# Kernel optimization log

Measured on AMD Instinct MI355X. Metric: run time of the kernel, lower is better.

## Reference

```python
import jax, jax.numpy as jnp
import numpy as np
from jax import lax

B = 4096
SRC = 50   # source_seq_len (encoder runs SRC-1 steps)
TGT = 25   # target_seq_len
R = 1024   # rnn_size
H = 67     # HUMAN_SIZE
I = 82     # input_size = 67 + 15 one-hot actions


def gru_cell(x, h, Wi, Wh, bi, bh):
    # torch.nn.GRUCell semantics; gate order (r, z, n); Wi:[3R,in], Wh:[3R,R]
    gi = x @ Wi.T + bi
    gh = h @ Wh.T + bh
    ir, iz, inn = jnp.split(gi, 3, axis=1)
    hr, hz, hn = jnp.split(gh, 3, axis=1)
    r = jax.nn.sigmoid(ir + hr)
    z = jax.nn.sigmoid(iz + hz)
    n = jnp.tanh(inn + r * hn)
    return (1.0 - z) * n + z * h


def setup_inputs() -> dict:
    key = jax.random.key(0)
    ks = jax.random.split(key, 12)
    s = 0.05
    return {
        "encoder_inputs": jax.random.normal(ks[0], (B, SRC - 1, I), jnp.float32),
        "decoder_inputs": jax.random.normal(ks[1], (B, TGT, I), jnp.float32),
        "Wi1": jax.random.normal(ks[2], (3 * R, I), jnp.float32) * s,
        "Wh1": jax.random.normal(ks[3], (3 * R, R), jnp.float32) * s,
        "bi1": jax.random.normal(ks[4], (3 * R,), jnp.float32) * s,
        "bh1": jax.random.normal(ks[5], (3 * R,), jnp.float32) * s,
        "Wi2": jax.random.normal(ks[6], (3 * R, R), jnp.float32) * s,
        "Wh2": jax.random.normal(ks[7], (3 * R, R), jnp.float32) * s,
        "bi2": jax.random.normal(ks[8], (3 * R,), jnp.float32) * s,
        "bh2": jax.random.normal(ks[9], (3 * R,), jnp.float32) * s,
        "Wfc": jax.random.normal(ks[10], (H, 2 * R), jnp.float32) * s,
        "bfc": jax.random.normal(ks[11], (H,), jnp.float32) * s,
        "use_cuda": 0,
    }


def reference(encoder_inputs, decoder_inputs, Wi1, Wh1, bi1, bh1,
              Wi2, Wh2, bi2, bh2, Wfc, bfc, use_cuda):
    # dropout=0.0 / eval mode -> dropout is identity (faithful to module defaults)
    bsz = encoder_inputs.shape[0]
    enc = jnp.transpose(encoder_inputs, (1, 0, 2))  # [SRC-1, B, I]
    dec = jnp.transpose(decoder_inputs, (1, 0, 2))  # [TGT,   B, I]

    s1 = jnp.zeros((bsz, R), encoder_inputs.dtype)
    s2 = jnp.zeros((bsz, R), encoder_inputs.dtype)

    def enc_step(carry, x):
        s1, s2 = carry
        s1 = gru_cell(x, s1, Wi1, Wh1, bi1, bh1)
        s2 = gru_cell(s1, s2, Wi2, Wh2, bi2, bh2)
        return (s1, s2), None

    (s1, s2), _ = lax.scan(enc_step, (s1, s2), enc)

    # decoder feeds back previous output (loop_function = identity on prev)
    prev0 = dec[0][:, :H]

    def dec_step(carry, dec_t):
        s1, s2, prev = carry
        inp = lax.stop_gradient(jnp.concatenate([prev, dec_t[:, H:]], axis=1))  # .detach()
        s1 = gru_cell(inp, s1, Wi1, Wh1, bi1, bh1)
        s2 = gru_cell(s1, s2, Wi2, Wh2, bi2, bh2)
        state_out = jnp.concatenate([s1, s2], axis=1)          # [B, 2R]
        out = inp[:, :H] + state_out @ Wfc.T + bfc             # residual velocities
        return (s1, s2, out), out

    _, outputs = lax.scan(dec_step, (s1, s2, prev0), dec)      # [TGT, B, H]
    return jnp.transpose(outputs, (1, 0, 2))                   # [B, TGT, H]
```

## Files before the change

### kernel.cpp

```cpp
#include <hip/hip_runtime.h>
#include <hip/hip_bf16.h>
#include <math.h>

#define B_        4096
#define ENC_STEPS 49
#define TGT_      25
#define R_        1024
#define H_        67
#define I_        82
#define IP_       96
#define IP2_      192
#define NG_       3072
#define FCN_      128
#define K2_       2048

typedef unsigned short u16;
typedef __attribute__((ext_vector_type(8))) short bf16x8_t;
typedef __attribute__((ext_vector_type(4))) float f32x4_t;

__device__ __forceinline__ float bf2f(u16 h) {
    union { unsigned int u; float f; } v; v.u = ((unsigned int)h) << 16; return v.f;
}
__device__ __forceinline__ u16 f2bf(float f) {
    union { unsigned int u; float f; } v; v.f = f;
    unsigned int u = v.u;
    u += 0x7fffu + ((u >> 16) & 1u);
    return (u16)(u >> 16);
}
__device__ __forceinline__ float sigmf(float x) { return 1.f / (1.f + __expf(-x)); }
__device__ __forceinline__ float tanhfast(float x) { return 1.f - 2.f / (__expf(2.f * x) + 1.f); }

__device__ __forceinline__ void g2l16(const u16* g, u16* l) {
    __builtin_amdgcn_global_load_lds(
        (const __attribute__((address_space(1))) unsigned int*)(const void*)g,
        (__attribute__((address_space(3))) unsigned int*)(void*)l,
        16, 0, 0);
}

__global__ void cast_bf16_kernel(const float* __restrict__ s, u16* __restrict__ d, int n) {
    int i = blockIdx.x * 256 + threadIdx.x;
    if (i < n) d[i] = f2bf(s[i]);
}
__global__ void pad_wi1_dup_kernel(const float* __restrict__ s, u16* __restrict__ d) {
    int i = blockIdx.x * 256 + threadIdx.x;
    if (i >= NG_ * IP2_) return;
    int r = i / IP2_, c = i % IP2_;
    int cc = (c < IP_) ? c : c - IP_;
    d[i] = (cc < I_) ? f2bf(s[r * I_ + cc]) : (u16)0;
}
__global__ void pad_wfc_kernel(const float* __restrict__ s, u16* __restrict__ d) {
    int i = blockIdx.x * 256 + threadIdx.x;
    if (i >= FCN_ * K2_) return;
    int r = i / K2_, c = i % K2_;
    d[i] = (r < H_) ? f2bf(s[r * K2_ + c]) : (u16)0;
}

__global__ void pad_all_x_kernel(const float* __restrict__ enc, u16* __restrict__ xall) {
    int i = blockIdx.x * 256 + threadIdx.x;
    if (i >= B_ * ENC_STEPS * IP_) return;
    int c = i % IP_;
    int t = (i / IP_) % ENC_STEPS;
    int b = i / (IP_ * ENC_STEPS);
    float v = (c < I_) ? enc[((size_t)b * ENC_STEPS + t) * I_ + c] : 0.f;
    u16 hi = f2bf(v);
    u16 lo = f2bf(v - bf2f(hi));
    size_t base = ((size_t)t * B_ + b) * IP2_;
    xall[base + c]       = hi;
    xall[base + IP_ + c] = lo;
}

__global__ void build_inp_kernel(const float* __restrict__ prev, int pstride,
                                 const float* __restrict__ dec, int t,
                                 u16* __restrict__ xpad) {
    int i = blockIdx.x * 256 + threadIdx.x;
    if (i >= B_ * IP_) return;
    int b = i / IP_, c = i % IP_;
    float v = 0.f;
    if (c < H_)      v = prev[(size_t)b * pstride + c];
    else if (c < I_) v = dec[((size_t)b * TGT_ + t) * I_ + c];
    u16 hi = f2bf(v);
    u16 lo = f2bf(v - bf2f(hi));
    xpad[(size_t)b * IP2_ + c]       = hi;
    xpad[(size_t)b * IP2_ + IP_ + c] = lo;
}

template<int KX>
__global__ __launch_bounds__(256, 2) void gru_step_kernel(
    const u16* __restrict__ Ax, int ldax,
    const u16* __restrict__ Wx,
    const u16* __restrict__ Ah, int ldah,
    const u16* __restrict__ Wh,
    const float* __restrict__ bi, const float* __restrict__ bh,
    float* __restrict__ hf,
    u16* __restrict__ hout)
{
    __shared__ __align__(16) u16 As[128 * 64];
    __shared__ __align__(16) u16 Ws[3 * 64 * 64];

    const int tid  = threadIdx.x;
    const int lane = tid & 63, wave = tid >> 6;
    const int wm = wave >> 1, wn = wave & 1;
    const int mbase = blockIdx.y * 128;
    const int nbase = blockIdx.x * 64;
    const int lr = lane & 15;
    const int swkey = lr & 7;

    constexpr int NX = KX / 64;
    constexpr int NH = R_ / 64;

    f32x4_t acc_r[4][2], acc_z[4][2], acc_xn[4][2], acc_hn[4][2];
#pragma unroll
    for (int i = 0; i < 4; i++)
#pragma unroll
        for (int j = 0; j < 2; j++) {
            acc_r[i][j]  = (f32x4_t){0,0,0,0};
            acc_z[i][j]  = (f32x4_t){0,0,0,0};
            acc_xn[i][j] = (f32x4_t){0,0,0,0};
            acc_hn[i][j] = (f32x4_t){0,0,0,0};
        }

    auto stage = [&](const u16* A, int lda, const u16* W, int ldw, int k0) {
#pragma unroll
        for (int p = 0; p < 4; p++) {
            int g = tid + p * 256;
            int row = g >> 3;
            int ch  = (g & 7) ^ (row & 7);
            g2l16(A + (size_t)(mbase + row) * lda + k0 + ch * 8, As + g * 8);
        }
#pragma unroll
        for (int p = 0; p < 6; p++) {
            int q = tid + p * 256;
            int row = q >> 3;
            int gate = row >> 6, rg = row & 63;
            int cw = (q & 7) ^ (row & 7);
            g2l16(W + ((size_t)gate * R_ + nbase + rg) * ldw + k0 + cw * 8, Ws + q * 8);
        }
    };

    auto compute = [&](bool xpass) {
#pragma unroll
        for (int kk = 0; kk < 2; kk++) {
            const int pos = ((kk * 4 + (lane >> 4)) ^ swkey) * 8;
            bf16x8_t a_f[4], w_r[2], w_z[2], w_n[2];
#pragma unroll
            for (int i = 0; i < 4; i++)
                a_f[i] = *(const bf16x8_t*)(As + (wm * 64 + i * 16 + lr) * 64 + pos);
#pragma unroll
            for (int j = 0; j < 2; j++) {
                int c = wn * 32 + j * 16 + lr;
                w_r[j] = *(const bf16x8_t*)(Ws + c * 64 + pos);
                w_z[j] = *(const bf16x8_t*)(Ws + (64 + c) * 64 + pos);
                w_n[j] = *(const bf16x8_t*)(Ws + (128 + c) * 64 + pos);
            }
            __builtin_amdgcn_s_setprio(1);
#pragma unroll
            for (int i = 0; i < 4; i++)
#pragma unroll
                for (int j = 0; j < 2; j++) {
                    acc_r[i][j] = __builtin_amdgcn_mfma_f32_16x16x32_bf16(a_f[i], w_r[j], acc_r[i][j], 0, 0, 0);
                    acc_z[i][j] = __builtin_amdgcn_mfma_f32_16x16x32_bf16(a_f[i], w_z[j], acc_z[i][j], 0, 0, 0);
                }
            if (xpass) {
#pragma unroll
                for (int i = 0; i < 4; i++)
#pragma unroll
                    for (int j = 0; j < 2; j++)
                        acc_xn[i][j] = __builtin_amdgcn_mfma_f32_16x16x32_bf16(a_f[i], w_n[j], acc_xn[i][j], 0, 0, 0);
            } else {
#pragma unroll
                for (int i = 0; i < 4; i++)
#pragma unroll
                    for (int j = 0; j < 2; j++)
                        acc_hn[i][j] = __builtin_amdgcn_mfma_f32_16x16x32_bf16(a_f[i], w_n[j], acc_hn[i][j], 0, 0, 0);
            }
            __builtin_amdgcn_s_setprio(0);
        }
    };

    for (int s = 0; s < NX; s++) {
        __syncthreads();
        stage(Ax, ldax, Wx, KX, s * 64);
        __syncthreads();
        compute(true);
    }
    for (int s = 0; s < NH; s++) {
        __syncthreads();
        stage(Ah, ldah, Wh, R_, s * 64);
        __syncthreads();
        compute(false);
    }

    const int rr2 = (lane >> 4) * 4;
#pragma unroll
    for (int j = 0; j < 2; j++) {
        const int col = nbase + wn * 32 + j * 16 + lr;
        const float b_ir = bi[col],          b_hr = bh[col];
        const float b_iz = bi[R_ + col],     b_hz = bh[R_ + col];
        const float b_in = bi[2 * R_ + col], b_hn = bh[2 * R_ + col];
#pragma unroll
        for (int i = 0; i < 4; i++) {
#pragma unroll
            for (int r = 0; r < 4; r++) {
                const int row = mbase + wm * 64 + i * 16 + rr2 + r;
                const float hold = hf[(size_t)row * R_ + col];
                const float rv = sigmf(acc_r[i][j][r] + b_ir + b_hr);
                const float zv = sigmf(acc_z[i][j][r] + b_iz + b_hz);
                const float nv = tanhfast(acc_xn[i][j][r] + b_in + rv * (acc_hn[i][j][r] + b_hn));
                const float hn = (1.f - zv) * nv + zv * hold;
                hf[(size_t)row * R_ + col] = hn;
                hout[(size_t)row * K2_ + col] = f2bf(hn);
            }
        }
    }
}

__global__ __launch_bounds__(256) void fc_part_kernel(
    const u16* __restrict__ A, const u16* __restrict__ W, float* __restrict__ part) {
    __shared__ __align__(16) u16 As[64 * 32];
    __shared__ __align__(16) u16 Bs[128 * 32];
    const int tid  = threadIdx.x;
    const int lane = tid & 63, wave = tid >> 6;
    const int wm = wave >> 1, wn = wave & 1;
    const int mbase = blockIdx.y * 64;
    const int kbase = blockIdx.x * 512;
    const int lr = lane & 15;
    const int sw = (((lane >> 4) ^ ((lr >> 1) & 3)) * 8);

    f32x4_t acc[2][4];
#pragma unroll
    for (int i = 0; i < 2; i++)
#pragma unroll
        for (int j = 0; j < 4; j++) acc[i][j] = (f32x4_t){0, 0, 0, 0};

    for (int k0 = 0; k0 < 512; k0 += 32) {
        __syncthreads();
        {
            int g = tid;
            int row = g >> 2;
            int ch  = (g & 3) ^ ((row >> 1) & 3);
            g2l16(A + (size_t)(mbase + row) * K2_ + kbase + k0 + ch * 8, As + g * 8);
        }
#pragma unroll
        for (int p = 0; p < 2; p++) {
            int q = tid + p * 256;
            int row = q >> 2;
            int cw  = (q & 3) ^ ((row >> 1) & 3);
            g2l16(W + (size_t)row * K2_ + kbase + k0 + cw * 8, Bs + q * 8);
        }
        __syncthreads();
        bf16x8_t a_f[2], b_f[4];
#pragma unroll
        for (int i = 0; i < 2; i++)
            a_f[i] = *(const bf16x8_t*)(As + (wm * 32 + i * 16 + lr) * 32 + sw);
#pragma unroll
        for (int j = 0; j < 4; j++)
            b_f[j] = *(const bf16x8_t*)(Bs + (wn * 64 + j * 16 + lr) * 32 + sw);
#pragma unroll
        for (int i = 0; i < 2; i++)
#pragma unroll
            for (int j = 0; j < 4; j++)
                acc[i][j] = __builtin_amdgcn_mfma_f32_16x16x32_bf16(a_f[i], b_f[j], acc[i][j], 0, 0, 0);
    }
    const int rr2 = (lane >> 4) * 4;
#pragma unroll
    for (int i = 0; i < 2; i++)
#pragma unroll
        for (int r = 0; r < 4; r++) {
            int row = mbase + wm * 32 + i * 16 + rr2 + r;
#pragma unroll
            for (int j = 0; j < 4; j++) {
                int col = wn * 64 + j * 16 + lr;
                part[((size_t)blockIdx.x * B_ + row) * FCN_ + col] = acc[i][j][r];
            }
        }
}

__global__ void fc_finish_kernel(const float* __restrict__ part, const float* __restrict__ prev,
                                 int pstride, const float* __restrict__ bfc,
                                 float* __restrict__ out, int t,
                                 const float* __restrict__ dec, u16* __restrict__ xpad,
                                 int write_x) {
    int i = blockIdx.x * 256 + threadIdx.x;
    if (i >= B_ * IP_) return;
    int b = i / IP_, c = i % IP_;
    float v = 0.f;
    if (c < H_) {
        size_t idx = (size_t)b * FCN_ + c;
        const size_t S = (size_t)B_ * FCN_;
        float s = (part[idx] + part[S + idx]) + (part[2 * S + idx] + part[3 * S + idx]);
        v = prev[(size_t)b * pstride + c] + s + bfc[c];
        out[((size_t)b * TGT_ + t) * H_ + c] = v;
    } else if (c < I_ && write_x) {
        v = dec[((size_t)b * TGT_ + (t + 1)) * I_ + c];
    }
    if (write_x) {
        u16 hi = f2bf(v);
        u16 lo = f2bf(v - bf2f(hi));
        xpad[(size_t)b * IP2_ + c]       = hi;
        xpad[(size_t)b * IP2_ + IP_ + c] = lo;
    }
}

extern "C" void kernel_launch(void* const* d_in, const int* in_sizes, int n_in,
                              void* d_out, int out_size, void* d_ws, size_t ws_size,
                              hipStream_t stream) {
    (void)in_sizes; (void)n_in; (void)out_size; (void)ws_size;
    const float* enc = (const float*)d_in[0];
    const float* dec = (const float*)d_in[1];
    const float* Wi1 = (const float*)d_in[2];
    const float* Wh1 = (const float*)d_in[3];
    const float* bi1 = (const float*)d_in[4];
    const float* bh1 = (const float*)d_in[5];
    const float* Wi2 = (const float*)d_in[6];
    const float* Wh2 = (const float*)d_in[7];
    const float* bi2 = (const float*)d_in[8];
    const float* bh2 = (const float*)d_in[9];
    const float* Wfc = (const float*)d_in[10];
    const float* bfc = (const float*)d_in[11];
    float* out = (float*)d_out;

    char* ws = (char*)d_ws;
    size_t off = 0;
    auto alloc = [&](size_t bytes) -> char* {
        char* p = ws + off;
        off += (bytes + 255) & ~(size_t)255;
        return p;
    };
    u16* Wh1b  = (u16*)alloc((size_t)NG_ * R_ * 2);
    u16* Wi2b  = (u16*)alloc((size_t)NG_ * R_ * 2);
    u16* Wh2b  = (u16*)alloc((size_t)NG_ * R_ * 2);
    u16* Wi1pb = (u16*)alloc((size_t)NG_ * IP2_ * 2);
    u16* Wfcb  = (u16*)alloc((size_t)FCN_ * K2_ * 2);
    u16* sbuf0 = (u16*)alloc((size_t)B_ * K2_ * 2);
    float* s1f = (float*)alloc((size_t)B_ * R_ * 4);
    float* s2f = (float*)alloc((size_t)B_ * R_ * 4);
    u16* sbuf1 = (u16*)alloc((size_t)B_ * K2_ * 2);
    u16* xall  = (u16*)alloc((size_t)ENC_STEPS * B_ * IP2_ * 2);
    u16* xpad2 = (u16*)alloc((size_t)B_ * IP2_ * 2);
    float* cfcp = (float*)alloc((size_t)4 * B_ * FCN_ * 4);
    u16* sbuf[2] = { sbuf0, sbuf1 };

    hipMemsetAsync(sbuf0, 0,
                   (size_t)B_ * K2_ * 2 + 2 * (size_t)B_ * R_ * 4, stream);

    cast_bf16_kernel<<<(NG_ * R_ + 255) / 256, 256, 0, stream>>>(Wh1, Wh1b, NG_ * R_);
    cast_bf16_kernel<<<(NG_ * R_ + 255) / 256, 256, 0, stream>>>(Wi2, Wi2b, NG_ * R_);
    cast_bf16_kernel<<<(NG_ * R_ + 255) / 256, 256, 0, stream>>>(Wh2, Wh2b, NG_ * R_);
    pad_wi1_dup_kernel<<<(NG_ * IP2_ + 255) / 256, 256, 0, stream>>>(Wi1, Wi1pb);
    pad_wfc_kernel<<<(FCN_ * K2_ + 255) / 256, 256, 0, stream>>>(Wfc, Wfcb);
    pad_all_x_kernel<<<(B_ * ENC_STEPS * IP_ + 255) / 256, 256, 0, stream>>>(enc, xall);

    dim3 gru_grid(R_ / 64, B_ / 128, 1);
    dim3 fc_grid(4, B_ / 64, 1);
    const int binp_blocks = (B_ * IP_ + 255) / 256;
    const int fcf_blocks  = (B_ * IP_ + 255) / 256;

    int phase = 0;

    for (int t = 0; t < ENC_STEPS; t++) {
        u16* cur = sbuf[phase];
        u16* nxt = sbuf[phase ^ 1];
        gru_step_kernel<IP2_><<<gru_grid, 256, 0, stream>>>(
            xall + (size_t)t * B_ * IP2_, IP2_, Wi1pb,
            cur, K2_, Wh1b, bi1, bh1, s1f, nxt);
        gru_step_kernel<R_><<<gru_grid, 256, 0, stream>>>(
            nxt, K2_, Wi2b,
            cur + R_, K2_, Wh2b, bi2, bh2, s2f, nxt + R_);
        phase ^= 1;
    }

    build_inp_kernel<<<binp_blocks, 256, 0, stream>>>(dec, TGT_ * I_, dec, 0, xpad2);
    for (int t = 0; t < TGT_; t++) {
        const float* prev;
        int pstride;
        if (t == 0) { prev = dec;                 pstride = TGT_ * I_; }
        else        { prev = out + (t - 1) * H_;  pstride = TGT_ * H_; }
        u16* cur = sbuf[phase];
        u16* nxt = sbuf[phase ^ 1];
        gru_step_kernel<IP2_><<<gru_grid, 256, 0, stream>>>(
            xpad2, IP2_, Wi1pb,
            cur, K2_, Wh1b, bi1, bh1, s1f, nxt);
        gru_step_kernel<R_><<<gru_grid, 256, 0, stream>>>(
            nxt, K2_, Wi2b,
            cur + R_, K2_, Wh2b, bi2, bh2, s2f, nxt + R_);
        fc_part_kernel<<<fc_grid, 256, 0, stream>>>(nxt, Wfcb, cfcp);
        fc_finish_kernel<<<fcf_blocks, 256, 0, stream>>>(
            cfcp, prev, pstride, bfc, out, t, dec, xpad2, (t < TGT_ - 1) ? 1 : 0);
        phase ^= 1;
    }
}
```

Baseline: 7.432 ms.

## Double-buffer GRU step LDS tiles with 256-row blocks and XCD-aware block swizzle

The GRU step kernel now uses 512 threads per block covering 256 batch rows, so each staged weight tile is reused by twice as many rows. LDS is double-buffered so the next k-slice is loaded while the current one is multiplied, which drops one barrier per iteration. The grid is flattened to 256 blocks with a swizzle that maps neighbouring blocks across XCDs. The trade-off is higher LDS use per block (about 112KB), fewer blocks in flight and a 256-block grid that may underfill the device.

```diff
diff --git a/kernel.cpp b/kernel.cpp
--- a/kernel.cpp
+++ b/kernel.cpp
@@ -85,7 +85,7 @@
 }
 
 template<int KX>
-__global__ __launch_bounds__(256, 2) void gru_step_kernel(
+__global__ __launch_bounds__(512, 2) void gru_step_kernel(
     const u16* __restrict__ Ax, int ldax,
     const u16* __restrict__ Wx,
     const u16* __restrict__ Ah, int ldah,
@@ -94,19 +94,22 @@
     float* __restrict__ hf,
     u16* __restrict__ hout)
 {
-    __shared__ __align__(16) u16 As[128 * 64];
-    __shared__ __align__(16) u16 Ws[3 * 64 * 64];
+    __shared__ __align__(16) u16 As[2][256 * 64];
+    __shared__ __align__(16) u16 Ws[2][3 * 64 * 64];
 
     const int tid  = threadIdx.x;
     const int lane = tid & 63, wave = tid >> 6;
     const int wm = wave >> 1, wn = wave & 1;
-    const int mbase = blockIdx.y * 128;
-    const int nbase = blockIdx.x * 64;
+    const int bid  = blockIdx.x;
+    const int swzb = (bid & 7) * 32 + (bid >> 3);
+    const int nbase = (swzb & 15) * 64;
+    const int mbase = (swzb >> 4) * 256;
     const int lr = lane & 15;
     const int swkey = lr & 7;
 
     constexpr int NX = KX / 64;
     constexpr int NH = R_ / 64;
+    constexpr int NT = NX + NH;
 
     f32x4_t acc_r[4][2], acc_z[4][2], acc_xn[4][2], acc_hn[4][2];
 #pragma unroll
@@ -119,38 +122,41 @@
             acc_hn[i][j] = (f32x4_t){0,0,0,0};
         }
 
-    auto stage = [&](const u16* A, int lda, const u16* W, int ldw, int k0) {
+    auto stage = [&](int s, int b) {
+        const u16* A; int lda; const u16* W; int ldw; int k0;
+        if (s < NX) { A = Ax; lda = ldax; W = Wx; ldw = KX; k0 = s * 64; }
+        else        { A = Ah; lda = ldah; W = Wh; ldw = R_;  k0 = (s - NX) * 64; }
 #pragma unroll
         for (int p = 0; p < 4; p++) {
-            int g = tid + p * 256;
+            int g = tid + p * 512;
             int row = g >> 3;
             int ch  = (g & 7) ^ (row & 7);
-            g2l16(A + (size_t)(mbase + row) * lda + k0 + ch * 8, As + g * 8);
-        }
-#pragma unroll
-        for (int p = 0; p < 6; p++) {
-            int q = tid + p * 256;
+            g2l16(A + (size_t)(mbase + row) * lda + k0 + ch * 8, As[b] + g * 8);
+        }
+#pragma unroll
+        for (int p = 0; p < 3; p++) {
+            int q = tid + p * 512;
             int row = q >> 3;
             int gate = row >> 6, rg = row & 63;
             int cw = (q & 7) ^ (row & 7);
-            g2l16(W + ((size_t)gate * R_ + nbase + rg) * ldw + k0 + cw * 8, Ws + q * 8);
+            g2l16(W + ((size_t)gate * R_ + nbase + rg) * ldw + k0 + cw * 8, Ws[b] + q * 8);
         }
     };
 
-    auto compute = [&](bool xpass) {
+    auto compute = [&](bool xpass, int b) {
 #pragma unroll
         for (int kk = 0; kk < 2; kk++) {
             const int pos = ((kk * 4 + (lane >> 4)) ^ swkey) * 8;
             bf16x8_t a_f[4], w_r[2], w_z[2], w_n[2];
 #pragma unroll
             for (int i = 0; i < 4; i++)
-                a_f[i] = *(const bf16x8_t*)(As + (wm * 64 + i * 16 + lr) * 64 + pos);
+                a_f[i] = *(const bf16x8_t*)(As[b] + (wm * 64 + i * 16 + lr) * 64 + pos);
 #pragma unroll
             for (int j = 0; j < 2; j++) {
                 int c = wn * 32 + j * 16 + lr;
-                w_r[j] = *(const bf16x8_t*)(Ws + c * 64 + pos);
-                w_z[j] = *(const bf16x8_t*)(Ws + (64 + c) * 64 + pos);
-                w_n[j] = *(const bf16x8_t*)(Ws + (128 + c) * 64 + pos);
+                w_r[j] = *(const bf16x8_t*)(Ws[b] + c * 64 + pos);
+                w_z[j] = *(const bf16x8_t*)(Ws[b] + (64 + c) * 64 + pos);
+                w_n[j] = *(const bf16x8_t*)(Ws[b] + (128 + c) * 64 + pos);
             }
             __builtin_amdgcn_s_setprio(1);
 #pragma unroll
@@ -177,17 +183,13 @@
         }
     };
 
-    for (int s = 0; s < NX; s++) {
+    stage(0, 0);
+    __syncthreads();
+#pragma unroll 1
+    for (int s = 0; s < NT; ++s) {
+        if (s + 1 < NT) stage(s + 1, (s + 1) & 1);
+        compute(s < NX, s & 1);
         __syncthreads();
-        stage(Ax, ldax, Wx, KX, s * 64);
-        __syncthreads();
-        compute(true);
-    }
-    for (int s = 0; s < NH; s++) {
-        __syncthreads();
-        stage(Ah, ldah, Wh, R_, s * 64);
-        __syncthreads();
-        compute(false);
     }
 
     const int rr2 = (lane >> 4) * 4;
@@ -350,7 +352,7 @@
     pad_wfc_kernel<<<(FCN_ * K2_ + 255) / 256, 256, 0, stream>>>(Wfc, Wfcb);
     pad_all_x_kernel<<<(B_ * ENC_STEPS * IP_ + 255) / 256, 256, 0, stream>>>(enc, xall);
 
-    dim3 gru_grid(R_ / 64, B_ / 128, 1);
+    dim3 gru_grid(256, 1, 1);
     dim3 fc_grid(4, B_ / 64, 1);
     const int binp_blocks = (B_ * IP_ + 255) / 256;
     const int fcf_blocks  = (B_ * IP_ + 255) / 256;
@@ -360,10 +362,10 @@
     for (int t = 0; t < ENC_STEPS; t++) {
         u16* cur = sbuf[phase];
         u16* nxt = sbuf[phase ^ 1];
-        gru_step_kernel<IP2_><<<gru_grid, 256, 0, stream>>>(
+        gru_step_kernel<IP2_><<<gru_grid, 512, 0, stream>>>(
             xall + (size_t)t * B_ * IP2_, IP2_, Wi1pb,
             cur, K2_, Wh1b, bi1, bh1, s1f, nxt);
-        gru_step_kernel<R_><<<gru_grid, 256, 0, stream>>>(
+        gru_step_kernel<R_><<<gru_grid, 512, 0, stream>>>(
             nxt, K2_, Wi2b,
             cur + R_, K2_, Wh2b, bi2, bh2, s2f, nxt + R_);
         phase ^= 1;
@@ -377,10 +379,10 @@
         else        { prev = out + (t - 1) * H_;  pstride = TGT_ * H_; }
         u16* cur = sbuf[phase];
         u16* nxt = sbuf[phase ^ 1];
-        gru_step_kernel<IP2_><<<gru_grid, 256, 0, stream>>>(
+        gru_step_kernel<IP2_><<<gru_grid, 512, 0, stream>>>(
             xpad2, IP2_, Wi1pb,
             cur, K2_, Wh1b, bi1, bh1, s1f, nxt);
-        gru_step_kernel<R_><<<gru_grid, 256, 0, stream>>>(
+        gru_step_kernel<R_><<<gru_grid, 512, 0, stream>>>(
             nxt, K2_, Wi2b,
             cur + R_, K2_, Wh2b, bi2, bh2, s2f, nxt + R_);
         fc_part_kernel<<<fc_grid, 256, 0, stream>>>(nxt, Wfcb, cfcp);
```

Measured after the change: 8.609 ms. 15.8% more time.

## Pre-pack GRU weights into MFMA fragment order and load directly to registers

Applied to the files above, without the earlier changes.

Weights are repacked once into a layout where each lane's 16-byte MFMA B-fragment is contiguous, so the GRU step kernel reads weight fragments straight from global memory into registers instead of staging them through LDS. This removes the LDS weight buffer and its shared-memory reads, which lowers LDS traffic and may raise occupancy. The costs are higher register pressure and more exposed global-load latency, since weight loads are issued before the barrier with no multi-stage pipelining. Each weight tile is now read separately by every wave instead of once per block.

```diff
diff --git a/kernel.cpp b/kernel.cpp
--- a/kernel.cpp
+++ b/kernel.cpp
@@ -37,22 +37,33 @@
         16, 0, 0);
 }
 
-__global__ void cast_bf16_kernel(const float* __restrict__ s, u16* __restrict__ d, int n) {
-    int i = blockIdx.x * 256 + threadIdx.x;
-    if (i < n) d[i] = f2bf(s[i]);
-}
-__global__ void pad_wi1_dup_kernel(const float* __restrict__ s, u16* __restrict__ d) {
+
+__global__ void pack_w1024_kernel(const float* __restrict__ s, u16* __restrict__ d) {
+    int i = blockIdx.x * 256 + threadIdx.x;
+    if (i >= NG_ * R_) return;
+    const int KQ = R_ / 32;
+    int e = i & 7, lane = (i >> 3) & 63, kq = (i >> 9) % KQ;
+    int ct = (i / (512 * KQ)) % 64, g = i / (512 * KQ * 64);
+    int row = g * R_ + ct * 16 + (lane & 15);
+    int k   = kq * 32 + (lane >> 4) * 8 + e;
+    d[i] = f2bf(s[(size_t)row * R_ + k]);
+}
+__global__ void pack_wi1_kernel(const float* __restrict__ s, u16* __restrict__ d) {
     int i = blockIdx.x * 256 + threadIdx.x;
     if (i >= NG_ * IP2_) return;
-    int r = i / IP2_, c = i % IP2_;
-    int cc = (c < IP_) ? c : c - IP_;
-    d[i] = (cc < I_) ? f2bf(s[r * I_ + cc]) : (u16)0;
+    const int KQ = IP2_ / 32;
+    int e = i & 7, lane = (i >> 3) & 63, kq = (i >> 9) % KQ;
+    int ct = (i / (512 * KQ)) % 64, g = i / (512 * KQ * 64);
+    int row = g * R_ + ct * 16 + (lane & 15);
+    int k   = kq * 32 + (lane >> 4) * 8 + e;
+    int cc  = (k < IP_) ? k : k - IP_;
+    d[i] = (cc < I_) ? f2bf(s[(size_t)row * I_ + cc]) : (u16)0;
 }
 __global__ void pad_wfc_kernel(const float* __restrict__ s, u16* __restrict__ d) {
     int i = blockIdx.x * 256 + threadIdx.x;
     if (i >= FCN_ * K2_) return;
     int r = i / K2_, c = i % K2_;
-    d[i] = (r < H_) ? f2bf(s[r * K2_ + c]) : (u16)0;
+    d[i] = (r < H_) ? f2bf(s[(size_t)r * K2_ + c]) : (u16)0;
 }
 
 __global__ void pad_all_x_kernel(const float* __restrict__ enc, u16* __restrict__ xall) {
@@ -87,15 +98,14 @@
 template<int KX>
 __global__ __launch_bounds__(256, 2) void gru_step_kernel(
     const u16* __restrict__ Ax, int ldax,
-    const u16* __restrict__ Wx,
+    const u16* __restrict__ Wxp,
     const u16* __restrict__ Ah, int ldah,
-    const u16* __restrict__ Wh,
+    const u16* __restrict__ Whp,
     const float* __restrict__ bi, const float* __restrict__ bh,
     float* __restrict__ hf,
     u16* __restrict__ hout)
 {
     __shared__ __align__(16) u16 As[128 * 64];
-    __shared__ __align__(16) u16 Ws[3 * 64 * 64];
 
     const int tid  = threadIdx.x;
     const int lane = tid & 63, wave = tid >> 6;
@@ -104,9 +114,11 @@
     const int nbase = blockIdx.x * 64;
     const int lr = lane & 15;
     const int swkey = lr & 7;
-
-    constexpr int NX = KX / 64;
-    constexpr int NH = R_ / 64;
+    const int ctb = (nbase >> 4) + wn * 2;
+
+    constexpr int NX  = KX / 64;
+    constexpr int NH  = R_ / 64;
+    constexpr int KQX = KX / 32;
 
     f32x4_t acc_r[4][2], acc_z[4][2], acc_xn[4][2], acc_hn[4][2];
 #pragma unroll
@@ -119,75 +131,91 @@
             acc_hn[i][j] = (f32x4_t){0,0,0,0};
         }
 
-    auto stage = [&](const u16* A, int lda, const u16* W, int ldw, int k0) {
-#pragma unroll
-        for (int p = 0; p < 4; p++) {
-            int g = tid + p * 256;
-            int row = g >> 3;
-            int ch  = (g & 7) ^ (row & 7);
-            g2l16(A + (size_t)(mbase + row) * lda + k0 + ch * 8, As + g * 8);
-        }
-#pragma unroll
-        for (int p = 0; p < 6; p++) {
-            int q = tid + p * 256;
-            int row = q >> 3;
-            int gate = row >> 6, rg = row & 63;
-            int cw = (q & 7) ^ (row & 7);
-            g2l16(W + ((size_t)gate * R_ + nbase + rg) * ldw + k0 + cw * 8, Ws + q * 8);
-        }
-    };
-
-    auto compute = [&](bool xpass) {
-#pragma unroll
-        for (int kk = 0; kk < 2; kk++) {
-            const int pos = ((kk * 4 + (lane >> 4)) ^ swkey) * 8;
-            bf16x8_t a_f[4], w_r[2], w_z[2], w_n[2];
-#pragma unroll
-            for (int i = 0; i < 4; i++)
-                a_f[i] = *(const bf16x8_t*)(As + (wm * 64 + i * 16 + lr) * 64 + pos);
-#pragma unroll
-            for (int j = 0; j < 2; j++) {
-                int c = wn * 32 + j * 16 + lr;
-                w_r[j] = *(const bf16x8_t*)(Ws + c * 64 + pos);
-                w_z[j] = *(const bf16x8_t*)(Ws + (64 + c) * 64 + pos);
-                w_n[j] = *(const bf16x8_t*)(Ws + (128 + c) * 64 + pos);
-            }
-            __builtin_amdgcn_s_setprio(1);
-#pragma unroll
-            for (int i = 0; i < 4; i++)
-#pragma unroll
-                for (int j = 0; j < 2; j++) {
-                    acc_r[i][j] = __builtin_amdgcn_mfma_f32_16x16x32_bf16(a_f[i], w_r[j], acc_r[i][j], 0, 0, 0);
-                    acc_z[i][j] = __builtin_amdgcn_mfma_f32_16x16x32_bf16(a_f[i], w_z[j], acc_z[i][j], 0, 0, 0);
+    {
+        const u16* wb[6];
+#pragma unroll
+        for (int g = 0; g < 3; g++)
+#pragma unroll
+            for (int j = 0; j < 2; j++)
+                wb[g * 2 + j] = Wxp + (size_t)((g * 64 + ctb + j) * KQX) * 512 + lane * 8;
+#pragma unroll 1
+        for (int s = 0; s < NX; s++) {
+            bf16x8_t w[2][6];
+#pragma unroll
+            for (int kk = 0; kk < 2; kk++)
+#pragma unroll
+                for (int u = 0; u < 6; u++)
+                    w[kk][u] = *(const bf16x8_t*)(wb[u] + (s * 2 + kk) * 512);
+            __syncthreads();
+#pragma unroll
+            for (int p = 0; p < 4; p++) {
+                int g = tid + p * 256, row = g >> 3, ch = (g & 7) ^ (row & 7);
+                g2l16(Ax + (size_t)(mbase + row) * ldax + s * 64 + ch * 8, As + g * 8);
+            }
+            __syncthreads();
+#pragma unroll
+            for (int kk = 0; kk < 2; kk++) {
+                const int pos = ((kk * 4 + (lane >> 4)) ^ swkey) * 8;
+                bf16x8_t a_f[4];
+#pragma unroll
+                for (int i = 0; i < 4; i++)
+                    a_f[i] = *(const bf16x8_t*)(As + (wm * 64 + i * 16 + lr) * 64 + pos);
+                __builtin_amdgcn_s_setprio(1);
+#pragma unroll
+                for (int i = 0; i < 4; i++) {
+                    acc_r[i][0]  = __builtin_amdgcn_mfma_f32_16x16x32_bf16(a_f[i], w[kk][0], acc_r[i][0], 0, 0, 0);
+                    acc_r[i][1]  = __builtin_amdgcn_mfma_f32_16x16x32_bf16(a_f[i], w[kk][1], acc_r[i][1], 0, 0, 0);
+                    acc_z[i][0]  = __builtin_amdgcn_mfma_f32_16x16x32_bf16(a_f[i], w[kk][2], acc_z[i][0], 0, 0, 0);
+                    acc_z[i][1]  = __builtin_amdgcn_mfma_f32_16x16x32_bf16(a_f[i], w[kk][3], acc_z[i][1], 0, 0, 0);
+                    acc_xn[i][0] = __builtin_amdgcn_mfma_f32_16x16x32_bf16(a_f[i], w[kk][4], acc_xn[i][0], 0, 0, 0);
+                    acc_xn[i][1] = __builtin_amdgcn_mfma_f32_16x16x32_bf16(a_f[i], w[kk][5], acc_xn[i][1], 0, 0, 0);
                 }
-            if (xpass) {
+                __builtin_amdgcn_s_setprio(0);
+            }
+        }
+    }
+    {
+        const u16* wb[6];
+#pragma unroll
+        for (int g = 0; g < 3; g++)
+#pragma unroll
+            for (int j = 0; j < 2; j++)
+                wb[g * 2 + j] = Whp + (size_t)((g * 64 + ctb + j) * 32) * 512 + lane * 8;
+#pragma unroll 1
+        for (int s = 0; s < NH; s++) {
+            bf16x8_t w[2][6];
+#pragma unroll
+            for (int kk = 0; kk < 2; kk++)
+#pragma unroll
+                for (int u = 0; u < 6; u++)
+                    w[kk][u] = *(const bf16x8_t*)(wb[u] + (s * 2 + kk) * 512);
+            __syncthreads();
+#pragma unroll
+            for (int p = 0; p < 4; p++) {
+                int g = tid + p * 256, row = g >> 3, ch = (g & 7) ^ (row & 7);
+                g2l16(Ah + (size_t)(mbase + row) * ldah + s * 64 + ch * 8, As + g * 8);
+            }
+            __syncthreads();
+#pragma unroll
+            for (int kk = 0; kk < 2; kk++) {
+                const int pos = ((kk * 4 + (lane >> 4)) ^ swkey) * 8;
+                bf16x8_t a_f[4];
 #pragma unroll
                 for (int i = 0; i < 4; i++)
-#pragma unroll
-                    for (int j = 0; j < 2; j++)
-                        acc_xn[i][j] = __builtin_amdgcn_mfma_f32_16x16x32_bf16(a_f[i], w_n[j], acc_xn[i][j], 0, 0, 0);
-            } else {
-#pragma unroll
-                for (int i = 0; i < 4; i++)
-#pragma unroll
-                    for (int j = 0; j < 2; j++)
-                        acc_hn[i][j] = __builtin_amdgcn_mfma_f32_16x16x32_bf16(a_f[i], w_n[j], acc_hn[i][j], 0, 0, 0);
-            }
-            __builtin_amdgcn_s_setprio(0);
-        }
-    };
-
-    for (int s = 0; s < NX; s++) {
-        __syncthreads();
-        stage(Ax, ldax, Wx, KX, s * 64);
-        __syncthreads();
-        compute(true);
-    }
-    for (int s = 0; s < NH; s++) {
-        __syncthreads();
-        stage(Ah, ldah, Wh, R_, s * 64);
-        __syncthreads();
-        compute(false);
+                    a_f[i] = *(const bf16x8_t*)(As + (wm * 64 + i * 16 + lr) * 64 + pos);
+                __builtin_amdgcn_s_setprio(1);
+#pragma unroll
+                for (int i = 0; i < 4; i++) {
+                    acc_r[i][0]  = __builtin_amdgcn_mfma_f32_16x16x32_bf16(a_f[i], w[kk][0], acc_r[i][0], 0, 0, 0);
+                    acc_r[i][1]  = __builtin_amdgcn_mfma_f32_16x16x32_bf16(a_f[i], w[kk][1], acc_r[i][1], 0, 0, 0);
+                    acc_z[i][0]  = __builtin_amdgcn_mfma_f32_16x16x32_bf16(a_f[i], w[kk][2], acc_z[i][0], 0, 0, 0);
+                    acc_z[i][1]  = __builtin_amdgcn_mfma_f32_16x16x32_bf16(a_f[i], w[kk][3], acc_z[i][1], 0, 0, 0);
+                    acc_hn[i][0] = __builtin_amdgcn_mfma_f32_16x16x32_bf16(a_f[i], w[kk][4], acc_hn[i][0], 0, 0, 0);
+                    acc_hn[i][1] = __builtin_amdgcn_mfma_f32_16x16x32_bf16(a_f[i], w[kk][5], acc_hn[i][1], 0, 0, 0);
+                }
+                __builtin_amdgcn_s_setprio(0);
+            }
+        }
     }
 
     const int rr2 = (lane >> 4) * 4;
@@ -326,10 +354,10 @@
         off += (bytes + 255) & ~(size_t)255;
         return p;
     };
-    u16* Wh1b  = (u16*)alloc((size_t)NG_ * R_ * 2);
-    u16* Wi2b  = (u16*)alloc((size_t)NG_ * R_ * 2);
-    u16* Wh2b  = (u16*)alloc((size_t)NG_ * R_ * 2);
-    u16* Wi1pb = (u16*)alloc((size_t)NG_ * IP2_ * 2);
+    u16* Wh1p  = (u16*)alloc((size_t)NG_ * R_ * 2);
+    u16* Wi2p  = (u16*)alloc((size_t)NG_ * R_ * 2);
+    u16* Wh2p  = (u16*)alloc((size_t)NG_ * R_ * 2);
+    u16* Wi1p  = (u16*)alloc((size_t)NG_ * IP2_ * 2);
     u16* Wfcb  = (u16*)alloc((size_t)FCN_ * K2_ * 2);
     u16* sbuf0 = (u16*)alloc((size_t)B_ * K2_ * 2);
     float* s1f = (float*)alloc((size_t)B_ * R_ * 4);
@@ -343,10 +371,10 @@
     hipMemsetAsync(sbuf0, 0,
                    (size_t)B_ * K2_ * 2 + 2 * (size_t)B_ * R_ * 4, stream);
 
-    cast_bf16_kernel<<<(NG_ * R_ + 255) / 256, 256, 0, stream>>>(Wh1, Wh1b, NG_ * R_);
-    cast_bf16_kernel<<<(NG_ * R_ + 255) / 256, 256, 0, stream>>>(Wi2, Wi2b, NG_ * R_);
-    cast_bf16_kernel<<<(NG_ * R_ + 255) / 256, 256, 0, stream>>>(Wh2, Wh2b, NG_ * R_);
-    pad_wi1_dup_kernel<<<(NG_ * IP2_ + 255) / 256, 256, 0, stream>>>(Wi1, Wi1pb);
+    pack_w1024_kernel<<<(NG_ * R_ + 255) / 256, 256, 0, stream>>>(Wh1, Wh1p);
+    pack_w1024_kernel<<<(NG_ * R_ + 255) / 256, 256, 0, stream>>>(Wi2, Wi2p);
+    pack_w1024_kernel<<<(NG_ * R_ + 255) / 256, 256, 0, stream>>>(Wh2, Wh2p);
+    pack_wi1_kernel<<<(NG_ * IP2_ + 255) / 256, 256, 0, stream>>>(Wi1, Wi1p);
     pad_wfc_kernel<<<(FCN_ * K2_ + 255) / 256, 256, 0, stream>>>(Wfc, Wfcb);
     pad_all_x_kernel<<<(B_ * ENC_STEPS * IP_ + 255) / 256, 256, 0, stream>>>(enc, xall);
 
@@ -361,11 +389,11 @@
         u16* cur = sbuf[phase];
         u16* nxt = sbuf[phase ^ 1];
         gru_step_kernel<IP2_><<<gru_grid, 256, 0, stream>>>(
-            xall + (size_t)t * B_ * IP2_, IP2_, Wi1pb,
-            cur, K2_, Wh1b, bi1, bh1, s1f, nxt);
+            xall + (size_t)t * B_ * IP2_, IP2_, Wi1p,
+            cur, K2_, Wh1p, bi1, bh1, s1f, nxt);
         gru_step_kernel<R_><<<gru_grid, 256, 0, stream>>>(
-            nxt, K2_, Wi2b,
-            cur + R_, K2_, Wh2b, bi2, bh2, s2f, nxt + R_);
+            nxt, K2_, Wi2p,
+            cur + R_, K2_, Wh2p, bi2, bh2, s2f, nxt + R_);
         phase ^= 1;
     }
 
@@ -378,11 +406,11 @@
         u16* cur = sbuf[phase];
         u16* nxt = sbuf[phase ^ 1];
         gru_step_kernel<IP2_><<<gru_grid, 256, 0, stream>>>(
-            xpad2, IP2_, Wi1pb,
-            cur, K2_, Wh1b, bi1, bh1, s1f, nxt);
+            xpad2, IP2_, Wi1p,
+            cur, K2_, Wh1p, bi1, bh1, s1f, nxt);
         gru_step_kernel<R_><<<gru_grid, 256, 0, stream>>>(
-            nxt, K2_, Wi2b,
-            cur + R_, K2_, Wh2b, bi2, bh2, s2f, nxt + R_);
+            nxt, K2_, Wi2p,
+            cur + R_, K2_, Wh2p, bi2, bh2, s2f, nxt + R_);
         fc_part_kernel<<<fc_grid, 256, 0, stream>>>(nxt, Wfcb, cfcp);
         fc_finish_kernel<<<fcf_blocks, 256, 0, stream>>>(
             cfcp, prev, pstride, bfc, out, t, dec, xpad2, (t < TGT_ - 1) ? 1 : 0);
```

Result: no change. 7.315 ms (-1.6%).
